# Optimization experiments

Measured on AMD Instinct MI355X. Metric: run time of the kernel, lower is better.

The kernel has to match this reference:

```python
import jax, jax.numpy as jnp
from jax import lax
import numpy as np

GAMMA = 0.25  # bottleneck commitment-loss weight (bn.gamma)
B, Q, N = 8, 64, 8192
K = 512       # n_quant_vecs (codebook size)
C = 256       # n_classes (mu-law quantization levels)


def setup_inputs() -> dict:
    key = jax.random.key(0)
    k1, k2, k3, k4 = jax.random.split(key, 4)
    ze = jax.random.normal(k1, (B, Q, N), dtype=jnp.float32)
    emb = jax.random.normal(k2, (K, Q), dtype=jnp.float32)
    quant_pred = jax.random.normal(k3, (B, C, N), dtype=jnp.float32)
    target_wav = jax.random.randint(k4, (B, N), 0, C, dtype=jnp.int64)
    return {"ze": ze, "emb": emb, "quant_pred": quant_pred, "target_wav": target_wav}


def reference(ze, emb, quant_pred, target_wav):
    # --- VQ codebook nearest-neighbor squared L2 distance ---
    # Original materializes (B,K,Q,N) diff; we use the expansion
    # ||z-e||^2 = ||z||^2 + ||e||^2 - 2 z.e to avoid the huge intermediate.
    ze2 = jnp.sum(ze * ze, axis=1)                       # (B,N)
    emb2 = jnp.sum(emb * emb, axis=1)                    # (K,)
    dots = jnp.einsum('bqn,kq->bkn', ze, emb)            # (B,K,N)
    d = ze2[:, None, :] + emb2[None, :, None] - 2.0 * dots  # (B,K,N)
    kmin = jnp.argmin(lax.stop_gradient(d), axis=1)      # (B,N)
    e_sel = emb[kmin]                                    # (B,N,Q) selected codewords
    ze_t = jnp.transpose(ze, (0, 2, 1))                  # (B,N,Q)

    # l2 loss: sg(ze) vs emb  -> gradient flows to codebook only
    l2_loss = jnp.sum((lax.stop_gradient(ze_t) - e_sel) ** 2, axis=-1)       # (B,N)
    # commitment loss: bn.min_dist uses sg(emb) -> gradient flows to ze only
    com_loss = GAMMA * jnp.sum((ze_t - lax.stop_gradient(e_sel)) ** 2, axis=-1)  # (B,N)

    # --- reconstruction CE: log-softmax over class dim + gather target ---
    log_pred = jax.nn.log_softmax(quant_pred, axis=1)    # (B,C,N)
    lp_t = jnp.take_along_axis(log_pred, target_wav[:, None, :], axis=1)[:, 0, :]  # (B,N)
    rec_loss = -lp_t

    total_loss = rec_loss.sum() + l2_loss.sum() + com_loss.sum()
    return total_loss
```

## Files before the change

### kernel.cpp

```cpp
#include <hip/hip_runtime.h>
#include <math.h>

#define GAMMA 0.25f
constexpr int B_ = 8, Q_ = 64, N_ = 8192, K_ = 512, C_ = 256;

typedef __attribute__((ext_vector_type(8))) short bf16x8;
typedef __attribute__((ext_vector_type(4))) short short4v;
typedef __attribute__((ext_vector_type(4))) float f32x4;

static __device__ inline short f2bf(float x) {
    union { float f; unsigned u; } v; v.f = x;
    unsigned r = (v.u + 0x7fffu + ((v.u >> 16) & 1u)) >> 16;
    return (short)r;
}
static __device__ inline float bf2f(short h) {
    union { unsigned u; float f; } v; v.u = ((unsigned)(unsigned short)h) << 16;
    return v.f;
}

__global__ __launch_bounds__(256) void prep_kernel(const float* __restrict__ emb,
                                                   short* __restrict__ embB,
                                                   float* __restrict__ e2g)
{
    const int r = blockIdx.x * 256 + threadIdx.x;
    if (r >= K_) return;
    const float4* src = (const float4*)(emb + r * Q_);
    short4v* dst = (short4v*)(embB + r * Q_);
    float s = 0.f;
    #pragma unroll
    for (int i = 0; i < 16; ++i) {
        const float4 v = src[i];
        short4v h;
        h[0] = f2bf(v.x); h[1] = f2bf(v.y); h[2] = f2bf(v.z); h[3] = f2bf(v.w);
        dst[i] = h;
        #pragma unroll
        for (int j = 0; j < 4; ++j) { const float a = bf2f(h[j]); s = fmaf(a, a, s); }
    }
    e2g[r] = s;
}

__global__ __launch_bounds__(256) void fused_kernel(
    const float* __restrict__ ze, const float* __restrict__ qp,
    const int* __restrict__ tgt, const short* __restrict__ embB,
    const float* __restrict__ e2g, float* __restrict__ out)
{
    __shared__ float smem[512];
    const int tid  = threadIdx.x;
    const int lane = tid & 63;
    const int w    = tid >> 6;
    const int n16  = lane & 15;
    const int quad = lane >> 4;
    const int g    = lane & 15;
    const int c0   = lane >> 4;

    const int base = blockIdx.x * 64;
    const int b    = base >> 13;
    const int n0   = base & (N_ - 1);
    const float* zb  = ze + (size_t)b * Q_ * N_;
    const float* qpb = qp + (size_t)b * C_ * N_;
    const float* qpn = qpb + n0 + g * 4;
    const int cbase  = w * 64 + c0 * 16;

    float4 ceA[8];
    #pragma unroll
    for (int j = 0; j < 8; ++j)
        ceA[j] = *(const float4*)(qpn + (size_t)(cbase + j) * N_);

    bf16x8 afrag[4][2];
    float zsq = 0.f;
    #pragma unroll
    for (int u = 0; u < 4; ++u) {
        const int nn = n0 + u * 16 + n16;
        #pragma unroll
        for (int s = 0; s < 2; ++s) {
            #pragma unroll
            for (int j = 0; j < 8; ++j) {
                const int q = s * 32 + quad * 8 + j;
                const float x = zb[(size_t)q * N_ + nn];
                zsq = fmaf(x, x, zsq);
                afrag[u][s][j] = f2bf(-2.f * x);
            }
        }
    }

    float4 ceB[8];
    #pragma unroll
    for (int j = 0; j < 8; ++j)
        ceB[j] = *(const float4*)(qpn + (size_t)(cbase + 8 + j) * N_);

    const short* bb = embB + (w * 128 + n16) * Q_ + quad * 8;
    bf16x8 Bv[8][2];
    float  e2v[8];
    #pragma unroll
    for (int t = 0; t < 8; ++t) {
        Bv[t][0] = *(const bf16x8*)(bb + t * 16 * Q_);
        Bv[t][1] = *(const bf16x8*)(bb + t * 16 * Q_ + 32);
        e2v[t]   = e2g[w * 128 + t * 16 + n16];
    }

    float xts[4] = {0.f, 0.f, 0.f, 0.f};
    if ((w == 1) && (lane < 16)) {
        #pragma unroll
        for (int j = 0; j < 4; ++j) {
            const int t = tgt[base + lane * 4 + j];
            xts[j] = qpb[(size_t)t * N_ + n0 + lane * 4 + j];
        }
    }

    f32x4 acc = {0.f, 0.f, 0.f, 0.f};
    #pragma unroll
    for (int j = 0; j < 8; ++j) {
        acc[0] += __expf(ceA[j].x); acc[1] += __expf(ceA[j].y);
        acc[2] += __expf(ceA[j].z); acc[3] += __expf(ceA[j].w);
    }
    #pragma unroll
    for (int j = 0; j < 8; ++j) {
        acc[0] += __expf(ceB[j].x); acc[1] += __expf(ceB[j].y);
        acc[2] += __expf(ceB[j].z); acc[3] += __expf(ceB[j].w);
    }
    #pragma unroll
    for (int r = 0; r < 4; ++r) {
        acc[r] += __shfl_xor(acc[r], 16, 64);
        acc[r] += __shfl_xor(acc[r], 32, 64);
    }
    if (c0 == 0) ((f32x4*)smem)[w * 16 + g] = acc;

    f32x4 best[4];
    #pragma unroll
    for (int u = 0; u < 4; ++u) best[u] = (f32x4){1e30f, 1e30f, 1e30f, 1e30f};

    #pragma unroll
    for (int t = 0; t < 8; ++t) {
        const f32x4 ce2 = {e2v[t], e2v[t], e2v[t], e2v[t]};
        #pragma unroll
        for (int u = 0; u < 4; ++u) {
            f32x4 a = __builtin_amdgcn_mfma_f32_16x16x32_bf16(afrag[u][0], Bv[t][0], ce2, 0, 0, 0);
            a       = __builtin_amdgcn_mfma_f32_16x16x32_bf16(afrag[u][1], Bv[t][1], a,   0, 0, 0);
            #pragma unroll
            for (int r = 0; r < 4; ++r) best[u][r] = fminf(best[u][r], a[r]);
        }
    }

    #pragma unroll
    for (int m = 1; m < 16; m <<= 1) {
        #pragma unroll
        for (int u = 0; u < 4; ++u) {
            #pragma unroll
            for (int r = 0; r < 4; ++r)
                best[u][r] = fminf(best[u][r], __shfl_xor(best[u][r], m, 64));
        }
    }
    if (n16 == 0) {
        #pragma unroll
        for (int u = 0; u < 4; ++u) {
            #pragma unroll
            for (int r = 0; r < 4; ++r)
                smem[256 + w * 64 + u * 16 + quad * 4 + r] = best[u][r];
        }
    }
    __syncthreads();

    if (w == 1) {
        float loss = 0.f;
        if (lane < 16) {
            const f32x4* part = (const f32x4*)smem;
            const f32x4 tot = (part[lane] + part[16 + lane]) +
                              (part[32 + lane] + part[48 + lane]);
            #pragma unroll
            for (int j = 0; j < 4; ++j) loss += __logf(tot[j]) - xts[j];
        }
        #pragma unroll
        for (int off = 32; off > 0; off >>= 1) loss += __shfl_down(loss, off, 64);
        if (lane == 0) atomicAdd(out, loss);
    }

    if (w == 0) {
        const float mn = fminf(fminf(smem[256 + lane], smem[256 + 64 + lane]),
                               fminf(smem[256 + 128 + lane], smem[256 + 192 + lane]));
        float val = 1.25f * (mn + zsq);
        #pragma unroll
        for (int off = 32; off > 0; off >>= 1) val += __shfl_down(val, off, 64);
        if (lane == 0) atomicAdd(out, val);
    }
}

extern "C" void kernel_launch(void* const* d_in, const int* in_sizes, int n_in,
                              void* d_out, int out_size, void* d_ws, size_t ws_size,
                              hipStream_t stream) {
    const float* ze  = (const float*)d_in[0];
    const float* emb = (const float*)d_in[1];
    const float* qp  = (const float*)d_in[2];
    const int*   tgt = (const int*)d_in[3];
    float* out = (float*)d_out;

    short* embB = (short*)d_ws;
    float* e2g  = (float*)((char*)d_ws + K_ * Q_ * sizeof(short));

    hipMemsetAsync(out, 0, sizeof(float), stream);

    prep_kernel<<<2, 256, 0, stream>>>(emb, embB, e2g);
    fused_kernel<<<1024, 256, 0, stream>>>(ze, qp, tgt, embB, e2g, out);
}
```

Baseline: 132.7 us.

## Split fused CE/VQ kernel into separate kernels with deterministic partial reduction

The single fused kernel, which did both the cross-entropy log-sum-exp and the VQ nearest-codeword search, is split into a dedicated CE kernel (2048 blocks of 32 columns, higher occupancy bound), a VQ kernel, and a final single-block reduce kernel. Per-block partial sums go to workspace instead of atomicAdd, which also removes the memset. The aim is to cut register pressure and let each phase reach better occupancy. The cost is extra kernel launches and serialising work that previously overlapped inside one block.

```diff
diff --git a/kernel.cpp b/kernel.cpp
--- a/kernel.cpp
+++ b/kernel.cpp
@@ -39,32 +39,84 @@
     e2g[r] = s;
 }
 
-__global__ __launch_bounds__(256) void fused_kernel(
-    const float* __restrict__ ze, const float* __restrict__ qp,
-    const int* __restrict__ tgt, const short* __restrict__ embB,
-    const float* __restrict__ e2g, float* __restrict__ out)
-{
-    __shared__ float smem[512];
+__global__ __launch_bounds__(256, 8) void ce_kernel(const float* __restrict__ qp,
+                                                    const int* __restrict__ tgt,
+                                                    float* __restrict__ cePart)
+{
+    __shared__ f32x4 parts[32];
+    const int tid  = threadIdx.x;
+    const int lane = tid & 63;
+    const int w    = tid >> 6;
+    const int g    = lane & 7;
+    const int c0   = lane >> 3;
+
+    const int base = blockIdx.x * 32;
+    const int b    = base >> 13;
+    const int n0   = base & (N_ - 1);
+    const float* qpb = qp + (size_t)b * C_ * N_;
+    const float* qpn = qpb + n0 + g * 4;
+    const int cbase  = w * 64 + c0 * 8;
+
+    float4 v[8];
+    #pragma unroll
+    for (int j = 0; j < 8; ++j)
+        v[j] = *(const float4*)(qpn + (size_t)(cbase + j) * N_);
+
+    float xts[4] = {0.f, 0.f, 0.f, 0.f};
+    if ((w == 0) && (lane < 8)) {
+        #pragma unroll
+        for (int j = 0; j < 4; ++j) {
+            const int t = tgt[base + lane * 4 + j];
+            xts[j] = qpb[(size_t)t * N_ + n0 + lane * 4 + j];
+        }
+    }
+
+    f32x4 acc = {0.f, 0.f, 0.f, 0.f};
+    #pragma unroll
+    for (int j = 0; j < 8; ++j) {
+        acc[0] += __expf(v[j].x); acc[1] += __expf(v[j].y);
+        acc[2] += __expf(v[j].z); acc[3] += __expf(v[j].w);
+    }
+    #pragma unroll
+    for (int r = 0; r < 4; ++r) {
+        acc[r] += __shfl_xor(acc[r], 8, 64);
+        acc[r] += __shfl_xor(acc[r], 16, 64);
+        acc[r] += __shfl_xor(acc[r], 32, 64);
+    }
+    if (c0 == 0) parts[w * 8 + g] = acc;
+    __syncthreads();
+
+    if (w == 0) {
+        float loss = 0.f;
+        if (lane < 8) {
+            const f32x4 tot = (parts[lane] + parts[8 + lane]) +
+                              (parts[16 + lane] + parts[24 + lane]);
+            #pragma unroll
+            for (int j = 0; j < 4; ++j) loss += __logf(tot[j]) - xts[j];
+        }
+        loss += __shfl_down(loss, 4, 64);
+        loss += __shfl_down(loss, 2, 64);
+        loss += __shfl_down(loss, 1, 64);
+        if (lane == 0) cePart[blockIdx.x] = loss;
+    }
+}
+
+__global__ __launch_bounds__(256) void vq_kernel(const float* __restrict__ ze,
+                                                 const short* __restrict__ embB,
+                                                 const float* __restrict__ e2g,
+                                                 float* __restrict__ vqPart)
+{
+    __shared__ float smem[256];
     const int tid  = threadIdx.x;
     const int lane = tid & 63;
     const int w    = tid >> 6;
     const int n16  = lane & 15;
     const int quad = lane >> 4;
-    const int g    = lane & 15;
-    const int c0   = lane >> 4;
 
     const int base = blockIdx.x * 64;
     const int b    = base >> 13;
     const int n0   = base & (N_ - 1);
-    const float* zb  = ze + (size_t)b * Q_ * N_;
-    const float* qpb = qp + (size_t)b * C_ * N_;
-    const float* qpn = qpb + n0 + g * 4;
-    const int cbase  = w * 64 + c0 * 16;
-
-    float4 ceA[8];
-    #pragma unroll
-    for (int j = 0; j < 8; ++j)
-        ceA[j] = *(const float4*)(qpn + (size_t)(cbase + j) * N_);
+    const float* zb = ze + (size_t)b * Q_ * N_;
 
     bf16x8 afrag[4][2];
     float zsq = 0.f;
@@ -83,11 +135,6 @@
         }
     }
 
-    float4 ceB[8];
-    #pragma unroll
-    for (int j = 0; j < 8; ++j)
-        ceB[j] = *(const float4*)(qpn + (size_t)(cbase + 8 + j) * N_);
-
     const short* bb = embB + (w * 128 + n16) * Q_ + quad * 8;
     bf16x8 Bv[8][2];
     float  e2v[8];
@@ -98,33 +145,6 @@
         e2v[t]   = e2g[w * 128 + t * 16 + n16];
     }
 
-    float xts[4] = {0.f, 0.f, 0.f, 0.f};
-    if ((w == 1) && (lane < 16)) {
-        #pragma unroll
-        for (int j = 0; j < 4; ++j) {
-            const int t = tgt[base + lane * 4 + j];
-            xts[j] = qpb[(size_t)t * N_ + n0 + lane * 4 + j];
-        }
-    }
-
-    f32x4 acc = {0.f, 0.f, 0.f, 0.f};
-    #pragma unroll
-    for (int j = 0; j < 8; ++j) {
-        acc[0] += __expf(ceA[j].x); acc[1] += __expf(ceA[j].y);
-        acc[2] += __expf(ceA[j].z); acc[3] += __expf(ceA[j].w);
-    }
-    #pragma unroll
-    for (int j = 0; j < 8; ++j) {
-        acc[0] += __expf(ceB[j].x); acc[1] += __expf(ceB[j].y);
-        acc[2] += __expf(ceB[j].z); acc[3] += __expf(ceB[j].w);
-    }
-    #pragma unroll
-    for (int r = 0; r < 4; ++r) {
-        acc[r] += __shfl_xor(acc[r], 16, 64);
-        acc[r] += __shfl_xor(acc[r], 32, 64);
-    }
-    if (c0 == 0) ((f32x4*)smem)[w * 16 + g] = acc;
-
     f32x4 best[4];
     #pragma unroll
     for (int u = 0; u < 4; ++u) best[u] = (f32x4){1e30f, 1e30f, 1e30f, 1e30f};
@@ -155,33 +175,37 @@
         for (int u = 0; u < 4; ++u) {
             #pragma unroll
             for (int r = 0; r < 4; ++r)
-                smem[256 + w * 64 + u * 16 + quad * 4 + r] = best[u][r];
+                smem[w * 64 + u * 16 + quad * 4 + r] = best[u][r];
         }
     }
     __syncthreads();
 
-    if (w == 1) {
-        float loss = 0.f;
-        if (lane < 16) {
-            const f32x4* part = (const f32x4*)smem;
-            const f32x4 tot = (part[lane] + part[16 + lane]) +
-                              (part[32 + lane] + part[48 + lane]);
-            #pragma unroll
-            for (int j = 0; j < 4; ++j) loss += __logf(tot[j]) - xts[j];
-        }
-        #pragma unroll
-        for (int off = 32; off > 0; off >>= 1) loss += __shfl_down(loss, off, 64);
-        if (lane == 0) atomicAdd(out, loss);
-    }
-
     if (w == 0) {
-        const float mn = fminf(fminf(smem[256 + lane], smem[256 + 64 + lane]),
-                               fminf(smem[256 + 128 + lane], smem[256 + 192 + lane]));
+        const float mn = fminf(fminf(smem[lane], smem[64 + lane]),
+                               fminf(smem[128 + lane], smem[192 + lane]));
         float val = 1.25f * (mn + zsq);
         #pragma unroll
         for (int off = 32; off > 0; off >>= 1) val += __shfl_down(val, off, 64);
-        if (lane == 0) atomicAdd(out, val);
-    }
+        if (lane == 0) vqPart[blockIdx.x] = val;
+    }
+}
+
+__global__ __launch_bounds__(256) void reduce_kernel(const float* __restrict__ cePart,
+                                                     const float* __restrict__ vqPart,
+                                                     float* __restrict__ out)
+{
+    __shared__ float sm[4];
+    const int tid = threadIdx.x;
+    float s = 0.f;
+    #pragma unroll
+    for (int i = 0; i < 8; ++i) s += cePart[tid + i * 256];
+    #pragma unroll
+    for (int i = 0; i < 4; ++i) s += vqPart[tid + i * 256];
+    #pragma unroll
+    for (int off = 32; off > 0; off >>= 1) s += __shfl_down(s, off, 64);
+    if ((tid & 63) == 0) sm[tid >> 6] = s;
+    __syncthreads();
+    if (tid == 0) out[0] = (sm[0] + sm[1]) + (sm[2] + sm[3]);
 }
 
 extern "C" void kernel_launch(void* const* d_in, const int* in_sizes, int n_in,
@@ -193,11 +217,13 @@
     const int*   tgt = (const int*)d_in[3];
     float* out = (float*)d_out;
 
-    short* embB = (short*)d_ws;
-    float* e2g  = (float*)((char*)d_ws + K_ * Q_ * sizeof(short));
-
-    hipMemsetAsync(out, 0, sizeof(float), stream);
-
+    short* embB   = (short*)d_ws;
+    float* e2g    = (float*)((char*)d_ws + 65536);
+    float* cePart = (float*)((char*)d_ws + 65536 + 2048);
+    float* vqPart = (float*)((char*)d_ws + 65536 + 2048 + 8192);
+
+    ce_kernel<<<2048, 256, 0, stream>>>(qp, tgt, cePart);
     prep_kernel<<<2, 256, 0, stream>>>(emb, embB, e2g);
-    fused_kernel<<<1024, 256, 0, stream>>>(ze, qp, tgt, embB, e2g, out);
-}
+    vq_kernel<<<1024, 256, 0, stream>>>(ze, embB, e2g, vqPart);
+    reduce_kernel<<<1, 256, 0, stream>>>(cePart, vqPart, out);
+}
```

After: 133.8 us. About the same (+0.8%).
